# Kernel tuning notes

Hardware: AMD Instinct MI355X
Metric: run time of the kernel (lower is better)

## Reference

```python
import jax, jax.numpy as jnp
import numpy as np

N_POINTS = 131072   # dense point cloud, batch['points'][0]
N_NODES = 2048      # coarse node set, batch['points'][-1]
NEIGHBOR_SEL = 32   # config['neighbor_sel']


def setup_inputs() -> dict:
    key = jax.random.key(0)
    k1, k2 = jax.random.split(key)
    point_cloud = jax.random.normal(k1, (N_POINTS, 3), dtype=jnp.float32)
    nodes = jax.random.normal(k2, (N_NODES, 3), dtype=jnp.float32)
    return {"point_cloud": point_cloud, "nodes": nodes, "neighbor_sel": NEIGHBOR_SEL}


def _knn1(points, nodes):
    # pairwise squared distances [N, M] = |p|^2 - 2 p.n + |n|^2
    d2 = (jnp.sum(points * points, axis=-1, keepdims=True)
          - 2.0 * (points @ nodes.T)
          + jnp.sum(nodes * nodes, axis=-1)[None, :])
    pcd_id = jnp.argmin(d2, axis=1)          # [N] nearest node per point (k=1 knn)
    min_d2 = jnp.min(d2, axis=1)             # [N] nearest squared distance
    return min_d2, pcd_id


def _grouping(pcd_id, n_nodes, k):
    # Replicates grouping_wrapper: for each node, collect the first k point
    # indices (in point order) assigned to it; unfilled slots stay -1.
    n = pcd_id.shape[0]
    order = jnp.argsort(pcd_id, stable=True)          # stable -> preserves point order within a node
    sorted_ids = pcd_id[order]                        # [N] non-decreasing node ids
    starts = jnp.searchsorted(sorted_ids, jnp.arange(n_nodes))  # group start offsets [M]
    rank = jnp.arange(n) - starts[sorted_ids]         # within-group rank of each point
    col = jnp.where(rank < k, rank, k)                # overflow slots routed to scratch column k
    patch = jnp.full((n_nodes, k + 1), -1, dtype=jnp.int32)
    patch = patch.at[sorted_ids, col].set(order.astype(jnp.int32))
    patch = patch[:, :k]                              # drop scratch column
    return jnp.maximum(patch, 0)                      # patch[patch < 0] = 0


def reference(point_cloud, nodes, neighbor_sel):
    min_d2, pcd_id = _knn1(point_cloud, nodes)
    patch = _grouping(pcd_id, nodes.shape[0], neighbor_sel)
    # pcd_id returned as [1, N, 1] matching knn(pc[None], nodes[None], k=1)
    return min_d2, pcd_id[None, :, None], patch[None]
```

## Files before the change

### kernel.cpp

```cpp
#include <hip/hip_runtime.h>
#include <hip/hip_bf16.h>

#define NPTS   131072
#define NNODES 2048
#define KSEL   32

#define TKNN   256
#define PPT    4
#define PPG_K  (TKNN * PPT)
#define NGRP_K (NPTS / PPG_K)
#define NCHUNK 16
#define CHN    (NNODES / NCHUNK)

#define GSZ    512
#define NG     (NPTS / GSZ)

typedef unsigned int uint;
typedef unsigned short u16;
typedef unsigned long long u64;
typedef float f2 __attribute__((ext_vector_type(2)));

__device__ __forceinline__ f2 splat(float s) { return (f2){s, s}; }

__device__ __forceinline__ uint f2ord(float d) {
    uint b = __float_as_uint(d);
    return (b & 0x80000000u) ? ~b : (b | 0x80000000u);
}
__device__ __forceinline__ float ord2f(uint t) {
    uint b = (t & 0x80000000u) ? (t ^ 0x80000000u) : ~t;
    return __uint_as_float(b);
}

__global__ __launch_bounds__(256) void prep_init(const float* __restrict__ nodes,
                                                 float4* __restrict__ n4,
                                                 u64* __restrict__ knnres) {
    int i = blockIdx.x * 256 + threadIdx.x;
    knnres[i] = ~0ull;
    if (i < NNODES) {
        float x = nodes[3 * i], y = nodes[3 * i + 1], z = nodes[3 * i + 2];
        float nn = __fadd_rn(__fadd_rn(__fmul_rn(x, x), __fmul_rn(y, y)), __fmul_rn(z, z));
        n4[i] = make_float4(x, y, z, nn);
    }
}

__global__ __launch_bounds__(256) void knn_part(const float* __restrict__ pts,
                                                const float4* __restrict__ n4,
                                                u64* __restrict__ knnres) {
    int bid = blockIdx.x;
    int c   = bid & (NCHUNK - 1);
    int g   = bid >> 4;
    int t   = threadIdx.x;

    f2 pp2[2], nx2[2], ny2[2], nz2[2];
    #pragma unroll
    for (int q = 0; q < 2; ++q) {
        #pragma unroll
        for (int h = 0; h < 2; ++h) {
            int pid = g * PPG_K + (2 * q + h) * TKNN + t;
            float p0 = pts[3 * pid], p1 = pts[3 * pid + 1], p2 = pts[3 * pid + 2];
            float pp = __fadd_rn(__fadd_rn(__fmul_rn(p0, p0), __fmul_rn(p1, p1)),
                                 __fmul_rn(p2, p2));
            pp2[q][h] = pp;
            nx2[q][h] = __fmul_rn(-2.0f, p0);
            ny2[q][h] = __fmul_rn(-2.0f, p1);
            nz2[q][h] = __fmul_rn(-2.0f, p2);
        }
    }

    const float4* np = n4 + c * CHN;
    float best[PPT];
    int   bi[PPT];
    #pragma unroll
    for (int q = 0; q < PPT; ++q) { best[q] = 3.4e38f; bi[q] = 0; }

    #pragma unroll 8
    for (int jj = 0; jj < CHN; ++jj) {
        float4 v = np[jj];
        #pragma unroll
        for (int q = 0; q < 2; ++q) {
            f2 m = nx2[q] * splat(v.x);
            f2 r = __builtin_elementwise_fma(ny2[q], splat(v.y), m);
            r    = __builtin_elementwise_fma(nz2[q], splat(v.z), r);
            f2 d = (pp2[q] + r) + splat(v.w);
            if (d.x < best[2*q])   { best[2*q]   = d.x; bi[2*q]   = jj; }
            if (d.y < best[2*q+1]) { best[2*q+1] = d.y; bi[2*q+1] = jj; }
        }
    }

    #pragma unroll
    for (int h = 0; h < PPT; ++h) {
        int pid = g * PPG_K + h * TKNN + t;
        u64 key = ((u64)f2ord(best[h]) << 32) | (uint)(c * CHN + bi[h]);
        atomicMin(&knnres[pid], key);
    }
}

__global__ __launch_bounds__(256) void merge_hist(const u64* __restrict__ knnres,
                                                  float* __restrict__ out_d2,
                                                  float* __restrict__ out_id,
                                                  int* __restrict__ pcd,
                                                  u16* __restrict__ hist16,
                                                  float* __restrict__ patch) {
    __shared__ uint lh[NNODES];
    int g = blockIdx.x, t = threadIdx.x;
    patch[(size_t)g * 256 + t] = 0.0f;
    for (int i = t; i < NNODES; i += 256) lh[i] = 0;
    __syncthreads();

    #pragma unroll
    for (int q = 0; q < GSZ / 256; ++q) {
        int pid = g * GSZ + q * 256 + t;
        u64 key = knnres[pid];
        uint bi = (uint)key;
        float d = ord2f((uint)(key >> 32));
        atomicAdd(&lh[bi], 1u);
        out_d2[pid] = d;
        out_id[pid] = (float)bi;
        pcd[pid]    = (int)bi;
    }
    __syncthreads();
    for (int i = t; i < NNODES; i += 256)
        hist16[(size_t)g * NNODES + i] = (u16)lh[i];
}

__global__ __launch_bounds__(256) void scan_offs(const u16* __restrict__ hist16,
                                                 uint* __restrict__ offs) {
    int t = threadIdx.x, lane = t & 63, wv = t >> 6;
    int node = blockIdx.x * 4 + wv;

    uint v0 = hist16[(size_t)(4 * lane + 0) * NNODES + node];
    uint v1 = hist16[(size_t)(4 * lane + 1) * NNODES + node];
    uint v2 = hist16[(size_t)(4 * lane + 2) * NNODES + node];
    uint v3 = hist16[(size_t)(4 * lane + 3) * NNODES + node];
    uint s = v0 + v1 + v2 + v3;
    uint a = s;
    #pragma unroll
    for (int d = 1; d < 64; d <<= 1) {
        uint y = __shfl_up(a, d, 64);
        if (lane >= d) a += y;
    }
    uint base = a - s;
    uint4 o = make_uint4(base, base + v0, base + v0 + v1, base + v0 + v1 + v2);
    *(uint4*)(offs + (size_t)node * NG + 4 * lane) = o;
}

__global__ __launch_bounds__(256) void scatter_patch(const int* __restrict__ pcd,
                                                     const uint* __restrict__ offs,
                                                     float* __restrict__ patch) {
    __shared__ int ids[GSZ];
    int g = blockIdx.x, t = threadIdx.x;
    ids[t]       = pcd[g * GSZ + t];
    ids[256 + t] = pcd[g * GSZ + 256 + t];
    __syncthreads();

    int i0 = t, i1 = 256 + t;
    int my0 = ids[i0], my1 = ids[i1];
    int r0 = 0, r1 = 0;
    #pragma unroll 8
    for (int j = 0; j < GSZ; ++j) {
        int id = ids[j];
        r0 += (j < i0 && id == my0) ? 1 : 0;
        r1 += (j < i1 && id == my1) ? 1 : 0;
    }
    uint rk0 = offs[(size_t)my0 * NG + g] + (uint)r0;
    uint rk1 = offs[(size_t)my1 * NG + g] + (uint)r1;
    if (rk0 < KSEL) patch[(size_t)my0 * KSEL + rk0] = (float)(g * GSZ + i0);
    if (rk1 < KSEL) patch[(size_t)my1 * KSEL + rk1] = (float)(g * GSZ + i1);
}

extern "C" void kernel_launch(void* const* d_in, const int* in_sizes, int n_in,
                              void* d_out, int out_size, void* d_ws, size_t ws_size,
                              hipStream_t stream) {
    const float* pts   = (const float*)d_in[0];
    const float* nodes = (const float*)d_in[1];

    float* out       = (float*)d_out;
    float* out_d2    = out;
    float* out_id    = out + NPTS;
    float* out_patch = out + 2 * NPTS;

    char* ws = (char*)d_ws;
    u64*   knnres = (u64*) ws;
    u16*   hist16 = (u16*) (ws + (1 << 20));
    uint*  offs   = (uint*) (ws + (2 << 20));
    int*   pcd    = (int*)  (ws + (4 << 20));
    float4* n4    = (float4*)(ws + (4 << 20) + (512 << 10));

    prep_init<<<NPTS / 256, 256, 0, stream>>>(nodes, n4, knnres);
    knn_part<<<NGRP_K * NCHUNK, TKNN, 0, stream>>>(pts, n4, knnres);
    merge_hist<<<NG, 256, 0, stream>>>(knnres, out_d2, out_id, pcd, hist16, out_patch);
    scan_offs<<<NNODES / 4, 256, 0, stream>>>(hist16, offs);
    scatter_patch<<<NG, 256, 0, stream>>>(pcd, offs, out_patch);
}
```

Before: 130.5 us.

## Track argmin per 4-node group with fminf and recompute exact index afterwards

The inner KNN loop now processes four nodes per step, reducing each point's best distance with a fminf chain and recording only the group base index. After the loop the winning group's four distances are recomputed to recover the exact node index, replacing per-node compare-and-select. The node chunk count is halved so each block scans twice as many nodes, with fewer partial atomicMin merges. The knnres init moves to hipMemsetAsync and node prep shrinks to a small kernel. Tie-breaking relies on the recomputed distances matching bitwise, and fminf can differ from the strict-less comparison on NaN or tied values.

New measurement: 120.5 us. 7.7% less time.

```diff
diff --git a/kernel.cpp b/kernel.cpp
--- a/kernel.cpp
+++ b/kernel.cpp
@@ -9,7 +9,7 @@
 #define PPT    4
 #define PPG_K  (TKNN * PPT)
 #define NGRP_K (NPTS / PPG_K)
-#define NCHUNK 16
+#define NCHUNK 8
 #define CHN    (NNODES / NCHUNK)
 
 #define GSZ    512
@@ -31,16 +31,12 @@
     return __uint_as_float(b);
 }
 
-__global__ __launch_bounds__(256) void prep_init(const float* __restrict__ nodes,
-                                                 float4* __restrict__ n4,
-                                                 u64* __restrict__ knnres) {
+__global__ __launch_bounds__(256) void prep_nodes(const float* __restrict__ nodes,
+                                                  float4* __restrict__ n4) {
     int i = blockIdx.x * 256 + threadIdx.x;
-    knnres[i] = ~0ull;
-    if (i < NNODES) {
-        float x = nodes[3 * i], y = nodes[3 * i + 1], z = nodes[3 * i + 2];
-        float nn = __fadd_rn(__fadd_rn(__fmul_rn(x, x), __fmul_rn(y, y)), __fmul_rn(z, z));
-        n4[i] = make_float4(x, y, z, nn);
-    }
+    float x = nodes[3 * i], y = nodes[3 * i + 1], z = nodes[3 * i + 2];
+    float nn = __fadd_rn(__fadd_rn(__fmul_rn(x, x), __fmul_rn(y, y)), __fmul_rn(z, z));
+    n4[i] = make_float4(x, y, z, nn);
 }
 
 __global__ __launch_bounds__(256) void knn_part(const float* __restrict__ pts,
@@ -48,7 +44,7 @@
                                                 u64* __restrict__ knnres) {
     int bid = blockIdx.x;
     int c   = bid & (NCHUNK - 1);
-    int g   = bid >> 4;
+    int g   = bid >> 3;
     int t   = threadIdx.x;
 
     f2 pp2[2], nx2[2], ny2[2], nz2[2];
@@ -69,28 +65,74 @@
 
     const float4* np = n4 + c * CHN;
     float best[PPT];
-    int   bi[PPT];
-    #pragma unroll
-    for (int q = 0; q < PPT; ++q) { best[q] = 3.4e38f; bi[q] = 0; }
-
-    #pragma unroll 8
-    for (int jj = 0; jj < CHN; ++jj) {
-        float4 v = np[jj];
+    int   qb[PPT];
+    #pragma unroll
+    for (int p = 0; p < PPT; ++p) { best[p] = 3.4e38f; qb[p] = 0; }
+
+    #pragma unroll 2
+    for (int jj = 0; jj < CHN; jj += 4) {
+        float4 v0 = np[jj + 0];
+        float4 v1 = np[jj + 1];
+        float4 v2 = np[jj + 2];
+        float4 v3 = np[jj + 3];
+
+        f2 d[2][4];
         #pragma unroll
         for (int q = 0; q < 2; ++q) {
-            f2 m = nx2[q] * splat(v.x);
-            f2 r = __builtin_elementwise_fma(ny2[q], splat(v.y), m);
-            r    = __builtin_elementwise_fma(nz2[q], splat(v.z), r);
-            f2 d = (pp2[q] + r) + splat(v.w);
-            if (d.x < best[2*q])   { best[2*q]   = d.x; bi[2*q]   = jj; }
-            if (d.y < best[2*q+1]) { best[2*q+1] = d.y; bi[2*q+1] = jj; }
-        }
-    }
-
-    #pragma unroll
-    for (int h = 0; h < PPT; ++h) {
-        int pid = g * PPG_K + h * TKNN + t;
-        u64 key = ((u64)f2ord(best[h]) << 32) | (uint)(c * CHN + bi[h]);
+            {   f2 m = nx2[q] * splat(v0.x);
+                f2 r = __builtin_elementwise_fma(ny2[q], splat(v0.y), m);
+                r    = __builtin_elementwise_fma(nz2[q], splat(v0.z), r);
+                d[q][0] = (pp2[q] + r) + splat(v0.w); }
+            {   f2 m = nx2[q] * splat(v1.x);
+                f2 r = __builtin_elementwise_fma(ny2[q], splat(v1.y), m);
+                r    = __builtin_elementwise_fma(nz2[q], splat(v1.z), r);
+                d[q][1] = (pp2[q] + r) + splat(v1.w); }
+            {   f2 m = nx2[q] * splat(v2.x);
+                f2 r = __builtin_elementwise_fma(ny2[q], splat(v2.y), m);
+                r    = __builtin_elementwise_fma(nz2[q], splat(v2.z), r);
+                d[q][2] = (pp2[q] + r) + splat(v2.w); }
+            {   f2 m = nx2[q] * splat(v3.x);
+                f2 r = __builtin_elementwise_fma(ny2[q], splat(v3.y), m);
+                r    = __builtin_elementwise_fma(nz2[q], splat(v3.z), r);
+                d[q][3] = (pp2[q] + r) + splat(v3.w); }
+        }
+
+        #pragma unroll
+        for (int p = 0; p < PPT; ++p) {
+            int q = p >> 1;
+            float e0 = (p & 1) ? d[q][0].y : d[q][0].x;
+            float e1 = (p & 1) ? d[q][1].y : d[q][1].x;
+            float e2 = (p & 1) ? d[q][2].y : d[q][2].x;
+            float e3 = (p & 1) ? d[q][3].y : d[q][3].x;
+            float m1 = fminf(fminf(best[p], e0), e1);
+            float nb = fminf(fminf(m1, e2), e3);
+            qb[p]   = (nb < best[p]) ? jj : qb[p];
+            best[p] = nb;
+        }
+    }
+
+    #pragma unroll
+    for (int p = 0; p < PPT; ++p) {
+        int q = p >> 1, h = p & 1;
+        float nx = nx2[q][h], ny = ny2[q][h], nz = nz2[q][h], pp = pp2[q][h];
+        float b  = best[p];
+        int base = qb[p];
+        float dd[4];
+        #pragma unroll
+        for (int o = 0; o < 4; ++o) {
+            float4 v = np[base + o];
+            float m = __fmul_rn(nx, v.x);
+            float r = __builtin_fmaf(ny, v.y, m);
+            r       = __builtin_fmaf(nz, v.z, r);
+            dd[o]   = __fadd_rn(__fadd_rn(pp, r), v.w);
+        }
+        int off = 3;
+        if (dd[2] == b) off = 2;
+        if (dd[1] == b) off = 1;
+        if (dd[0] == b) off = 0;
+
+        int pid = g * PPG_K + p * TKNN + t;
+        u64 key = ((u64)f2ord(b) << 32) | (uint)(c * CHN + base + off);
         atomicMin(&knnres[pid], key);
     }
 }
@@ -186,7 +228,8 @@
     int*   pcd    = (int*)  (ws + (4 << 20));
     float4* n4    = (float4*)(ws + (4 << 20) + (512 << 10));
 
-    prep_init<<<NPTS / 256, 256, 0, stream>>>(nodes, n4, knnres);
+    hipMemsetAsync(knnres, 0xFF, (size_t)NPTS * sizeof(u64), stream);
+    prep_nodes<<<NNODES / 256, 256, 0, stream>>>(nodes, n4);
     knn_part<<<NGRP_K * NCHUNK, TKNN, 0, stream>>>(pts, n4, knnres);
     merge_hist<<<NG, 256, 0, stream>>>(knnres, out_d2, out_id, pcd, hist16, out_patch);
     scan_offs<<<NNODES / 4, 256, 0, stream>>>(hist16, offs);
```

## Split node chunk into two interleaved halves with quad-granular min tracking

Applied to the files above, without the earlier changes.

The KNN inner loop now tracks only a running fminf per group of four nodes and two independent halves of the chunk, recording the quad index instead of the exact node index per compare. The exact argmin within the winning quad is recovered afterward by recomputing four distances. Points per thread drop from 4 to 2 and chunks from 16 to 8, so there are twice as many nodes per block and the same total block count. The aim is to cut compare/select instructions and lengthen dependency chains less, at the cost of a small recompute epilogue and reliance on bit-exact recomputation for tie detection.

New measurement: 119.5 us. -8.4%, faster.

```diff
diff --git a/kernel.cpp b/kernel.cpp
--- a/kernel.cpp
+++ b/kernel.cpp
@@ -6,11 +6,12 @@
 #define KSEL   32
 
 #define TKNN   256
-#define PPT    4
+#define PPT    2
 #define PPG_K  (TKNN * PPT)
 #define NGRP_K (NPTS / PPG_K)
-#define NCHUNK 16
+#define NCHUNK 8
 #define CHN    (NNODES / NCHUNK)
+#define HALF   (CHN / 2)
 
 #define GSZ    512
 #define NG     (NPTS / GSZ)
@@ -48,49 +49,120 @@
                                                 u64* __restrict__ knnres) {
     int bid = blockIdx.x;
     int c   = bid & (NCHUNK - 1);
-    int g   = bid >> 4;
+    int g   = bid >> 3;
     int t   = threadIdx.x;
 
-    f2 pp2[2], nx2[2], ny2[2], nz2[2];
-    #pragma unroll
-    for (int q = 0; q < 2; ++q) {
+    f2 pp2, nx2, ny2, nz2;
+    #pragma unroll
+    for (int h = 0; h < 2; ++h) {
+        int pid = g * PPG_K + h * TKNN + t;
+        float p0 = pts[3 * pid], p1 = pts[3 * pid + 1], p2 = pts[3 * pid + 2];
+        float pp = __fadd_rn(__fadd_rn(__fmul_rn(p0, p0), __fmul_rn(p1, p1)),
+                             __fmul_rn(p2, p2));
+        pp2[h] = pp;
+        nx2[h] = __fmul_rn(-2.0f, p0);
+        ny2[h] = __fmul_rn(-2.0f, p1);
+        nz2[h] = __fmul_rn(-2.0f, p2);
+    }
+
+    const float4* np = n4 + c * CHN;
+    float bestA[PPT], bestB[PPT];
+    int   qbA[PPT],   qbB[PPT];
+    #pragma unroll
+    for (int p = 0; p < PPT; ++p) {
+        bestA[p] = 3.4e38f; bestB[p] = 3.4e38f; qbA[p] = 0; qbB[p] = 0;
+    }
+
+    #pragma unroll 2
+    for (int jj = 0; jj < HALF; jj += 4) {
+        float4 a0 = np[jj + 0];
+        float4 a1 = np[jj + 1];
+        float4 a2 = np[jj + 2];
+        float4 a3 = np[jj + 3];
+        float4 b0 = np[HALF + jj + 0];
+        float4 b1 = np[HALF + jj + 1];
+        float4 b2 = np[HALF + jj + 2];
+        float4 b3 = np[HALF + jj + 3];
+
+        f2 dA0, dA1, dA2, dA3, dB0, dB1, dB2, dB3;
+        {   f2 m = nx2 * splat(a0.x);
+            f2 r = __builtin_elementwise_fma(ny2, splat(a0.y), m);
+            r    = __builtin_elementwise_fma(nz2, splat(a0.z), r);
+            dA0  = (pp2 + r) + splat(a0.w); }
+        {   f2 m = nx2 * splat(a1.x);
+            f2 r = __builtin_elementwise_fma(ny2, splat(a1.y), m);
+            r    = __builtin_elementwise_fma(nz2, splat(a1.z), r);
+            dA1  = (pp2 + r) + splat(a1.w); }
+        {   f2 m = nx2 * splat(a2.x);
+            f2 r = __builtin_elementwise_fma(ny2, splat(a2.y), m);
+            r    = __builtin_elementwise_fma(nz2, splat(a2.z), r);
+            dA2  = (pp2 + r) + splat(a2.w); }
+        {   f2 m = nx2 * splat(a3.x);
+            f2 r = __builtin_elementwise_fma(ny2, splat(a3.y), m);
+            r    = __builtin_elementwise_fma(nz2, splat(a3.z), r);
+            dA3  = (pp2 + r) + splat(a3.w); }
+        {   f2 m = nx2 * splat(b0.x);
+            f2 r = __builtin_elementwise_fma(ny2, splat(b0.y), m);
+            r    = __builtin_elementwise_fma(nz2, splat(b0.z), r);
+            dB0  = (pp2 + r) + splat(b0.w); }
+        {   f2 m = nx2 * splat(b1.x);
+            f2 r = __builtin_elementwise_fma(ny2, splat(b1.y), m);
+            r    = __builtin_elementwise_fma(nz2, splat(b1.z), r);
+            dB1  = (pp2 + r) + splat(b1.w); }
+        {   f2 m = nx2 * splat(b2.x);
+            f2 r = __builtin_elementwise_fma(ny2, splat(b2.y), m);
+            r    = __builtin_elementwise_fma(nz2, splat(b2.z), r);
+            dB2  = (pp2 + r) + splat(b2.w); }
+        {   f2 m = nx2 * splat(b3.x);
+            f2 r = __builtin_elementwise_fma(ny2, splat(b3.y), m);
+            r    = __builtin_elementwise_fma(nz2, splat(b3.z), r);
+            dB3  = (pp2 + r) + splat(b3.w); }
+
         #pragma unroll
-        for (int h = 0; h < 2; ++h) {
-            int pid = g * PPG_K + (2 * q + h) * TKNN + t;
-            float p0 = pts[3 * pid], p1 = pts[3 * pid + 1], p2 = pts[3 * pid + 2];
-            float pp = __fadd_rn(__fadd_rn(__fmul_rn(p0, p0), __fmul_rn(p1, p1)),
-                                 __fmul_rn(p2, p2));
-            pp2[q][h] = pp;
-            nx2[q][h] = __fmul_rn(-2.0f, p0);
-            ny2[q][h] = __fmul_rn(-2.0f, p1);
-            nz2[q][h] = __fmul_rn(-2.0f, p2);
+        for (int p = 0; p < PPT; ++p) {
+            float eA0 = p ? dA0.y : dA0.x;
+            float eA1 = p ? dA1.y : dA1.x;
+            float eA2 = p ? dA2.y : dA2.x;
+            float eA3 = p ? dA3.y : dA3.x;
+            float mA  = fminf(fminf(bestA[p], eA0), eA1);
+            float nA  = fminf(fminf(mA, eA2), eA3);
+            qbA[p]    = (nA < bestA[p]) ? jj : qbA[p];
+            bestA[p]  = nA;
+
+            float eB0 = p ? dB0.y : dB0.x;
+            float eB1 = p ? dB1.y : dB1.x;
+            float eB2 = p ? dB2.y : dB2.x;
+            float eB3 = p ? dB3.y : dB3.x;
+            float mB  = fminf(fminf(bestB[p], eB0), eB1);
+            float nB  = fminf(fminf(mB, eB2), eB3);
+            qbB[p]    = (nB < bestB[p]) ? jj : qbB[p];
+            bestB[p]  = nB;
         }
     }
 
-    const float4* np = n4 + c * CHN;
-    float best[PPT];
-    int   bi[PPT];
-    #pragma unroll
-    for (int q = 0; q < PPT; ++q) { best[q] = 3.4e38f; bi[q] = 0; }
-
-    #pragma unroll 8
-    for (int jj = 0; jj < CHN; ++jj) {
-        float4 v = np[jj];
+    #pragma unroll
+    for (int p = 0; p < PPT; ++p) {
+        float bA = bestA[p], bB = bestB[p];
+        float b  = fminf(bA, bB);
+        int base = (bB < bA) ? (HALF + qbB[p]) : qbA[p];
+
+        float nx = nx2[p], ny = ny2[p], nz = nz2[p], pp = pp2[p];
+        float dd[4];
         #pragma unroll
-        for (int q = 0; q < 2; ++q) {
-            f2 m = nx2[q] * splat(v.x);
-            f2 r = __builtin_elementwise_fma(ny2[q], splat(v.y), m);
-            r    = __builtin_elementwise_fma(nz2[q], splat(v.z), r);
-            f2 d = (pp2[q] + r) + splat(v.w);
-            if (d.x < best[2*q])   { best[2*q]   = d.x; bi[2*q]   = jj; }
-            if (d.y < best[2*q+1]) { best[2*q+1] = d.y; bi[2*q+1] = jj; }
+        for (int o = 0; o < 4; ++o) {
+            float4 v = np[base + o];
+            float m = __fmul_rn(nx, v.x);
+            float r = __builtin_fmaf(ny, v.y, m);
+            r       = __builtin_fmaf(nz, v.z, r);
+            dd[o]   = __fadd_rn(__fadd_rn(pp, r), v.w);
         }
-    }
-
-    #pragma unroll
-    for (int h = 0; h < PPT; ++h) {
-        int pid = g * PPG_K + h * TKNN + t;
-        u64 key = ((u64)f2ord(best[h]) << 32) | (uint)(c * CHN + bi[h]);
+        int off = 3;
+        if (dd[2] == b) off = 2;
+        if (dd[1] == b) off = 1;
+        if (dd[0] == b) off = 0;
+
+        int pid = g * PPG_K + p * TKNN + t;
+        u64 key = ((u64)f2ord(b) << 32) | (uint)(c * CHN + base + off);
         atomicMin(&knnres[pid], key);
     }
 }
```
